# Kernel tuning notes

Measured on AMD Instinct MI355X. Metric: run time of the kernel, lower is better.

The kernel has to match this reference:

```python
import jax, jax.numpy as jnp
import numpy as np

B, IN, H, OUT = 8192, 1024, 1024, 512


def setup_inputs() -> dict:
    key = jax.random.key(0)
    ks = jax.random.split(key, 13)
    s_in = 1.0 / np.sqrt(IN + H)
    s_h = 1.0 / np.sqrt(H)
    return {
        "x": jax.random.normal(ks[0], (B, IN), jnp.float32),
        "h": jax.random.normal(ks[1], (B, H), jnp.float32),
        "c": jax.random.normal(ks[2], (B, H), jnp.float32),
        "Wi": jax.random.normal(ks[3], (IN + H, H), jnp.float32) * s_in,
        "bi": jax.random.normal(ks[4], (H,), jnp.float32) * s_in,
        "Wf": jax.random.normal(ks[5], (IN + H, H), jnp.float32) * s_in,
        "bf": jax.random.normal(ks[6], (H,), jnp.float32) * s_in,
        "Wo": jax.random.normal(ks[7], (IN + H, H), jnp.float32) * s_in,
        "bo": jax.random.normal(ks[8], (H,), jnp.float32) * s_in,
        "Wc": jax.random.normal(ks[9], (IN + H, H), jnp.float32) * s_in,
        "bc": jax.random.normal(ks[10], (H,), jnp.float32) * s_in,
        "Wy": jax.random.normal(ks[11], (H, OUT), jnp.float32) * s_h,
        "by": jax.random.normal(ks[12], (OUT,), jnp.float32) * s_h,
    }


def reference(x, h, c, Wi, bi, Wf, bf, Wo, bo, Wc, bc, Wy, by):
    # combined: [B, IN+H]
    combined = jnp.concatenate([x, h], axis=1)
    # Fuse the four gate matmuls into one [B, IN+H] x [IN+H, 4H] GEMM.
    W_all = jnp.concatenate([Wi, Wf, Wo, Wc], axis=1)        # [IN+H, 4H]
    b_all = jnp.concatenate([bi, bf, bo, bc], axis=0)        # [4H]
    gates = combined @ W_all + b_all                          # [B, 4H]
    gi, gf, go, gc = jnp.split(gates, 4, axis=1)
    i_t = jax.nn.sigmoid(gi)
    f_t = jax.nn.sigmoid(gf)
    o_t = jax.nn.sigmoid(go)
    c_tilde = jnp.tanh(gc)
    c_new = f_t * c + i_t * c_tilde
    h_new = o_t * jnp.tanh(c_new)
    y_hat = h_new @ Wy + by                                   # [B, OUT]
    return (y_hat, (h_new, c_new))
```

## Files before the change

### kernel.cpp

```cpp
#include <hip/hip_runtime.h>
#include <hip/hip_bf16.h>
#include <stdint.h>

#define B_ 8192
#define IN_ 1024
#define H_ 1024
#define OUT_ 512
#define KC 2048
#define N4 4096

typedef __bf16 bf16_t;
typedef __bf16 bf16x8 __attribute__((ext_vector_type(8)));
typedef float f32x4 __attribute__((ext_vector_type(4)));

__device__ __forceinline__ void gload_lds16(const void* g, void* l) {
  __builtin_amdgcn_global_load_lds(
      (const __attribute__((address_space(1))) uint32_t*)g,
      (__attribute__((address_space(3))) uint32_t*)l, 16, 0, 0);
}

__device__ __forceinline__ float fsigmoid(float x) {
  return __builtin_amdgcn_rcpf(1.0f + __expf(-x));
}
__device__ __forceinline__ float ftanh(float x) {
  return 2.0f * __builtin_amdgcn_rcpf(1.0f + __expf(-2.0f * x)) - 1.0f;
}


__global__ __launch_bounds__(256) void pack_combined(
    const float* __restrict__ x, const float* __restrict__ h,
    bf16_t* __restrict__ out) {
  const int row = blockIdx.x;
  const int j = threadIdx.x * 8;
  const float* src = (j < IN_) ? (x + (size_t)row * IN_ + j)
                               : (h + (size_t)row * H_ + (j - IN_));
  float4 a = ((const float4*)src)[0];
  float4 b = ((const float4*)src)[1];
  bf16x8 v;
  v[0] = (bf16_t)a.x; v[1] = (bf16_t)a.y; v[2] = (bf16_t)a.z; v[3] = (bf16_t)a.w;
  v[4] = (bf16_t)b.x; v[5] = (bf16_t)b.y; v[6] = (bf16_t)b.z; v[7] = (bf16_t)b.w;
  *(bf16x8*)(out + (size_t)row * KC + j) = v;
}

__global__ __launch_bounds__(256) void transpose_pack(
    const float* __restrict__ src, bf16_t* __restrict__ dst, int K, int N,
    int RS, int RO) {
  __shared__ float tile[64][65];
  const int k0 = blockIdx.y * 64, n0 = blockIdx.x * 64;
  const int t = threadIdx.x;
  const int tr = t >> 4, tc4 = (t & 15) * 4;
#pragma unroll
  for (int r = 0; r < 4; ++r) {
    const int k = tr + r * 16;
    float4 v = *(const float4*)(src + (size_t)(k0 + k) * N + n0 + tc4);
    tile[k][tc4] = v.x; tile[k][tc4 + 1] = v.y;
    tile[k][tc4 + 2] = v.z; tile[k][tc4 + 3] = v.w;
  }
  __syncthreads();
  const int nr = t >> 3, kc8 = (t & 7) * 8;
#pragma unroll
  for (int r = 0; r < 2; ++r) {
    const int n = nr + r * 32;
    bf16x8 v;
#pragma unroll
    for (int q = 0; q < 8; ++q) v[q] = (bf16_t)tile[kc8 + q][n];
    *(bf16x8*)(dst + (size_t)((n0 + n) * RS + RO) * K + k0 + kc8) = v;
  }
}

__global__ __launch_bounds__(512) void gemm1_8ph(
    const bf16_t* __restrict__ A, const bf16_t* __restrict__ Bt,
    const float* __restrict__ c_in,
    const float* __restrict__ bi, const float* __restrict__ bfg,
    const float* __restrict__ bo, const float* __restrict__ bc,
    float* __restrict__ h_out, float* __restrict__ c_out,
    bf16_t* __restrict__ hb) {
  constexpr int K = KC;
  constexpr int NT = K / 64;
  __shared__ char lds[131072];

  const int tid = threadIdx.x;
  const int lane = tid & 63;
  const int w = tid >> 6;
  const int wr = w >> 2, wc = w & 3;
  const int l15 = lane & 15, l4 = lane >> 4;

  const int wg = blockIdx.x;
  const int swz = (wg & 7) * 64 + (wg >> 3);
  const int bx = swz >> 5;
  const int by = swz & 31;
  const int m0 = by * 256, n0 = bx * 256;

  const int jrow = lane >> 2;
  const int jcol = ((lane & 3) * 16) ^ ((lane >> 5) << 5);
  const char* Asrc = (const char*)A + (size_t)(m0 + w * 16 + jrow) * (K * 2) + jcol;
  const char* Bsrc = (const char*)Bt + (size_t)(n0 + w * 16 + jrow) * (K * 2) + jcol;
  char* ldsA = lds;
  char* ldsB = lds + 32768;
  const int wchunk = w * 2048;

#define STG_A(buf, h, tt) do {                                            \
    gload_lds16(Asrc + (size_t)(h) * 128 * (K * 2) + (size_t)(tt) * 128,  \
                ldsA + (buf) * 65536 + (h) * 16384 + wchunk);             \
    gload_lds16(Asrc + (size_t)(h) * 128 * (K * 2) + (size_t)(tt) * 128 + 64, \
                ldsA + (buf) * 65536 + (h) * 16384 + wchunk + 1024);      \
  } while (0)
#define STG_B(buf, h, tt) do {                                            \
    gload_lds16(Bsrc + (size_t)(h) * 128 * (K * 2) + (size_t)(tt) * 128,  \
                ldsB + (buf) * 65536 + (h) * 16384 + wchunk);             \
    gload_lds16(Bsrc + (size_t)(h) * 128 * (K * 2) + (size_t)(tt) * 128 + 64, \
                ldsB + (buf) * 65536 + (h) * 16384 + wchunk + 1024);      \
  } while (0)

  const int rdoff = l15 * 64 + ((l4 * 16) ^ ((l15 >> 3) << 5));
  const char* ldsArd = lds + wr * 16384 + rdoff;
  const char* ldsBrd = lds + 32768 + (wc >> 1) * 16384 + (wc & 1) * 8192 + rdoff;

  f32x4 acc[8][4] = {};
  bf16x8 fa[4][2], fb[4][2];

#define MFMA_Q(MIBASE, NIBASE)                                                \
  do {                                                                        \
    __builtin_amdgcn_s_setprio(1);                                            \
    _Pragma("unroll") for (int kk = 0; kk < 2; ++kk)                          \
        _Pragma("unroll") for (int mi = 0; mi < 4; ++mi)                      \
            _Pragma("unroll") for (int ni = 0; ni < 2; ++ni)                  \
                acc[(MIBASE) + mi][(NIBASE) + ni] =                           \
                    __builtin_amdgcn_mfma_f32_16x16x32_bf16(                  \
                        fa[mi][kk], fb[(NIBASE) + ni][kk],                    \
                        acc[(MIBASE) + mi][(NIBASE) + ni], 0, 0, 0);          \
    __builtin_amdgcn_s_setprio(0);                                            \
  } while (0)

  STG_B(0, 0, 0); STG_A(0, 0, 0); STG_A(0, 1, 0); STG_B(0, 1, 0);
  STG_B(1, 0, 1); STG_A(1, 0, 1); STG_A(1, 1, 1);
  asm volatile("s_waitcnt vmcnt(6)" ::: "memory");
  __builtin_amdgcn_s_barrier();

  for (int t = 0; t < NT; ++t) {
    const int buf = t & 1;
    const int nbuf = buf ^ 1;
    const char* ard = ldsArd + buf * 65536;
    const char* brd = ldsBrd + buf * 65536;
    const bool st1 = (t + 1 < NT);
    const bool st2 = (t + 2 < NT);

#pragma unroll
    for (int mi = 0; mi < 4; ++mi)
#pragma unroll
      for (int kk = 0; kk < 2; ++kk)
        fa[mi][kk] = *(const bf16x8*)(ard + mi * 2048 + kk * 1024);
#pragma unroll
    for (int ni = 0; ni < 2; ++ni)
#pragma unroll
      for (int kk = 0; kk < 2; ++kk)
        fb[ni][kk] = *(const bf16x8*)(brd + ni * 2048 + kk * 1024);
    if (st1) STG_B(nbuf, 1, t + 1);
    __builtin_amdgcn_s_barrier();
    MFMA_Q(0, 0);
    __builtin_amdgcn_s_barrier();

#pragma unroll
    for (int ni = 2; ni < 4; ++ni)
#pragma unroll
      for (int kk = 0; kk < 2; ++kk)
        fb[ni][kk] = *(const bf16x8*)(brd + ni * 2048 + kk * 1024);
    __builtin_amdgcn_s_barrier();
    MFMA_Q(0, 2);
    __builtin_amdgcn_s_barrier();

#pragma unroll
    for (int mi = 0; mi < 4; ++mi)
#pragma unroll
      for (int kk = 0; kk < 2; ++kk)
        fa[mi][kk] = *(const bf16x8*)(ard + (mi + 4) * 2048 + kk * 1024);
    if (st2) STG_B(buf, 0, t + 2);
    __builtin_amdgcn_s_barrier();
    MFMA_Q(4, 0);
    __builtin_amdgcn_s_barrier();

    if (st2) { STG_A(buf, 0, t + 2); STG_A(buf, 1, t + 2); }
    __builtin_amdgcn_s_barrier();
    MFMA_Q(4, 2);
    if (st2) asm volatile("s_waitcnt vmcnt(6)" ::: "memory");
    else     asm volatile("s_waitcnt vmcnt(0)" ::: "memory");
    __builtin_amdgcn_s_barrier();
  }

  const int hc0 = n0 >> 2;
  float* ldsF = (float*)lds;
  const int ehc = tid & 63;
  const int err0 = (tid >> 6) * 8;
  const float bI = bi[hc0 + ehc];
  const float bF = bfg[hc0 + ehc];
  const float bO = bo[hc0 + ehc];
  const float bC = bc[hc0 + ehc];

  for (int ch = 0; ch < 4; ++ch) {
    __builtin_amdgcn_s_barrier();
    if (wr == (ch >> 1)) {
      const int mib = (ch & 1) * 4;
#pragma unroll
      for (int mi = 0; mi < 4; ++mi)
#pragma unroll
        for (int ni = 0; ni < 4; ++ni) {
          const int col = wc * 64 + ni * 16 + l15;
          const int hc = col >> 2, g = col & 3;
#pragma unroll
          for (int q = 0; q < 4; ++q) {
            const int rr = mi * 16 + l4 * 4 + q;
            ldsF[rr * 256 + ((hc ^ rr) * 4) + g] = acc[mib + mi][ni][q];
          }
        }
    }
    __builtin_amdgcn_s_barrier();
#pragma unroll
    for (int r = 0; r < 8; ++r) {
      const int rr = err0 + r;
      f32x4 gq = *(const f32x4*)&ldsF[rr * 256 + ((ehc ^ rr) * 4)];
      const size_t gidx = (size_t)(m0 + ch * 64 + rr) * H_ + hc0 + ehc;
      float I = fsigmoid(gq[0] + bI);
      float F = fsigmoid(gq[1] + bF);
      float O = fsigmoid(gq[2] + bO);
      float Ct = ftanh(gq[3] + bC);
      float cn = F * c_in[gidx] + I * Ct;
      float hn = O * ftanh(cn);
      c_out[gidx] = cn;
      h_out[gidx] = hn;
      hb[gidx] = (bf16_t)hn;
    }
  }
#undef STG_A
#undef STG_B
#undef MFMA_Q
}

__global__ __launch_bounds__(256) void gemm_bt_f32(
    const bf16_t* __restrict__ A, const bf16_t* __restrict__ Bt,
    float* __restrict__ Cout, const float* __restrict__ bias,
    int M, int N, int K) {
  __shared__ bf16_t As[128 * 64];
  __shared__ bf16_t Bs[128 * 64];
  const int tid = threadIdx.x;
  const int lane = tid & 63;
  const int wave = tid >> 6;
  const int m0 = blockIdx.y * 128;
  const int n0 = blockIdx.x * 128;
  const int wr = wave >> 1, wc = wave & 1;
  const int l15 = lane & 15, l4 = lane >> 4;

  f32x4 acc[4][4] = {};

  const int srow = tid >> 3;
  const int skel = (tid & 7) * 8;
  const size_t aBase = (size_t)(m0 + srow) * K + skel;
  const size_t bBase = (size_t)(n0 + srow) * K + skel;
  char* aL = (char*)As + wave * 1024;
  char* bL = (char*)Bs + wave * 1024;

  for (int kt = 0; kt < K; kt += 64) {
    __syncthreads();
#pragma unroll
    for (int i = 0; i < 4; ++i) {
      gload_lds16(A + aBase + (size_t)i * 32 * K + kt, aL + i * 4096);
      gload_lds16(Bt + bBase + (size_t)i * 32 * K + kt, bL + i * 4096);
    }
    __syncthreads();
#pragma unroll
    for (int kk = 0; kk < 2; ++kk) {
      bf16x8 af[4], bq[4];
#pragma unroll
      for (int mi = 0; mi < 4; ++mi)
        af[mi] = *(const bf16x8*)((const char*)As +
                 (wr * 64 + mi * 16 + l15) * 128 + kk * 64 + l4 * 16);
#pragma unroll
      for (int ni = 0; ni < 4; ++ni)
        bq[ni] = *(const bf16x8*)((const char*)Bs +
                 (wc * 64 + ni * 16 + l15) * 128 + kk * 64 + l4 * 16);
#pragma unroll
      for (int mi = 0; mi < 4; ++mi)
#pragma unroll
        for (int ni = 0; ni < 4; ++ni)
          acc[mi][ni] = __builtin_amdgcn_mfma_f32_16x16x32_bf16(
              af[mi], bq[ni], acc[mi][ni], 0, 0, 0);
    }
  }

  const int col = n0 + wc * 64 + l15;
  const int row0 = m0 + wr * 64 + l4 * 4;
#pragma unroll
  for (int ni = 0; ni < 4; ++ni) {
    const float bv = bias[col + ni * 16];
#pragma unroll
    for (int mi = 0; mi < 4; ++mi)
#pragma unroll
      for (int q = 0; q < 4; ++q)
        Cout[(size_t)(row0 + mi * 16 + q) * N + col + ni * 16] =
            acc[mi][ni][q] + bv;
  }
}

extern "C" void kernel_launch(void* const* d_in, const int* in_sizes, int n_in,
                              void* d_out, int out_size, void* d_ws,
                              size_t ws_size, hipStream_t stream) {
  const float* x = (const float*)d_in[0];
  const float* h = (const float*)d_in[1];
  const float* c = (const float*)d_in[2];
  const float* Wi = (const float*)d_in[3];
  const float* bi = (const float*)d_in[4];
  const float* Wf = (const float*)d_in[5];
  const float* bfg = (const float*)d_in[6];
  const float* Wo = (const float*)d_in[7];
  const float* bo = (const float*)d_in[8];
  const float* Wc = (const float*)d_in[9];
  const float* bc = (const float*)d_in[10];
  const float* Wy = (const float*)d_in[11];
  const float* by = (const float*)d_in[12];

  char* ws = (char*)d_ws;
  bf16_t* combined = (bf16_t*)ws;
  bf16_t* Wt = (bf16_t*)(ws + 33554432);
  bf16_t* Wyt = (bf16_t*)(ws + 33554432 + 16777216);
  bf16_t* hb = (bf16_t*)(ws + 33554432 + 16777216 + 1048576);

  float* y_out = (float*)d_out;
  float* h_out = y_out + (size_t)B_ * OUT_;
  float* c_out = h_out + (size_t)B_ * H_;

  pack_combined<<<dim3(B_), dim3(256), 0, stream>>>(x, h, combined);
  const float* Wg[4] = {Wi, Wf, Wo, Wc};
  for (int g = 0; g < 4; ++g)
    transpose_pack<<<dim3(H_ / 64, KC / 64), dim3(256), 0, stream>>>(
        Wg[g], Wt, KC, H_, 4, g);
  transpose_pack<<<dim3(OUT_ / 64, H_ / 64), dim3(256), 0, stream>>>(
      Wy, Wyt, H_, OUT_, 1, 0);

  gemm1_8ph<<<dim3((B_ / 256) * (N4 / 256)), dim3(512), 0, stream>>>(
      combined, Wt, c, bi, bfg, bo, bc, h_out, c_out, hb);

  gemm_bt_f32<<<dim3(OUT_ / 128, B_ / 128), dim3(256), 0, stream>>>(
      hb, Wyt, y_out, by, B_, OUT_, H_);
}
```

Before: 212.2 us.

## Simplify GEMM1 main loop to a single-stage prefetch and merge gate transposes

Replaces the 8-phase, barrier-heavy ping-pong schedule in the main gate GEMM with a simpler loop. Each iteration reads all A/B fragments from LDS, issues every global-to-LDS load for the next tile, runs 64 MFMAs in two halves, then waits for the loads and does one barrier. This removes the many intra-iteration barriers and the two-tile-ahead staging, at the cost of less fine-grained overlap and more fragment registers held at once. It also fuses the four per-gate weight transpose launches into a single 3D-grid launch to cut launch overhead.

```diff
diff --git a/kernel.cpp b/kernel.cpp
--- a/kernel.cpp
+++ b/kernel.cpp
@@ -42,9 +42,37 @@
   *(bf16x8*)(out + (size_t)row * KC + j) = v;
 }
 
+__global__ __launch_bounds__(256) void transpose_pack4(
+    const float* __restrict__ Wi, const float* __restrict__ Wf,
+    const float* __restrict__ Wo, const float* __restrict__ Wc,
+    bf16_t* __restrict__ dst) {
+  const int g = blockIdx.z;
+  const float* src = (g == 0) ? Wi : (g == 1) ? Wf : (g == 2) ? Wo : Wc;
+  __shared__ float tile[64][65];
+  const int k0 = blockIdx.y * 64, n0 = blockIdx.x * 64;
+  const int t = threadIdx.x;
+  const int tr = t >> 4, tc4 = (t & 15) * 4;
+#pragma unroll
+  for (int r = 0; r < 4; ++r) {
+    const int k = tr + r * 16;
+    float4 v = *(const float4*)(src + (size_t)(k0 + k) * H_ + n0 + tc4);
+    tile[k][tc4] = v.x; tile[k][tc4 + 1] = v.y;
+    tile[k][tc4 + 2] = v.z; tile[k][tc4 + 3] = v.w;
+  }
+  __syncthreads();
+  const int nr = t >> 3, kc8 = (t & 7) * 8;
+#pragma unroll
+  for (int r = 0; r < 2; ++r) {
+    const int n = nr + r * 32;
+    bf16x8 v;
+#pragma unroll
+    for (int q = 0; q < 8; ++q) v[q] = (bf16_t)tile[kc8 + q][n];
+    *(bf16x8*)(dst + (size_t)((n0 + n) * 4 + g) * KC + k0 + kc8) = v;
+  }
+}
+
 __global__ __launch_bounds__(256) void transpose_pack(
-    const float* __restrict__ src, bf16_t* __restrict__ dst, int K, int N,
-    int RS, int RO) {
+    const float* __restrict__ src, bf16_t* __restrict__ dst, int K, int N) {
   __shared__ float tile[64][65];
   const int k0 = blockIdx.y * 64, n0 = blockIdx.x * 64;
   const int t = threadIdx.x;
@@ -64,7 +92,7 @@
     bf16x8 v;
 #pragma unroll
     for (int q = 0; q < 8; ++q) v[q] = (bf16_t)tile[kc8 + q][n];
-    *(bf16x8*)(dst + (size_t)((n0 + n) * RS + RO) * K + k0 + kc8) = v;
+    *(bf16x8*)(dst + (size_t)(n0 + n) * K + k0 + kc8) = v;
   }
 }
 
@@ -117,24 +145,10 @@
   const char* ldsBrd = lds + 32768 + (wc >> 1) * 16384 + (wc & 1) * 8192 + rdoff;
 
   f32x4 acc[8][4] = {};
-  bf16x8 fa[4][2], fb[4][2];
-
-#define MFMA_Q(MIBASE, NIBASE)                                                \
-  do {                                                                        \
-    __builtin_amdgcn_s_setprio(1);                                            \
-    _Pragma("unroll") for (int kk = 0; kk < 2; ++kk)                          \
-        _Pragma("unroll") for (int mi = 0; mi < 4; ++mi)                      \
-            _Pragma("unroll") for (int ni = 0; ni < 2; ++ni)                  \
-                acc[(MIBASE) + mi][(NIBASE) + ni] =                           \
-                    __builtin_amdgcn_mfma_f32_16x16x32_bf16(                  \
-                        fa[mi][kk], fb[(NIBASE) + ni][kk],                    \
-                        acc[(MIBASE) + mi][(NIBASE) + ni], 0, 0, 0);          \
-    __builtin_amdgcn_s_setprio(0);                                            \
-  } while (0)
-
-  STG_B(0, 0, 0); STG_A(0, 0, 0); STG_A(0, 1, 0); STG_B(0, 1, 0);
-  STG_B(1, 0, 1); STG_A(1, 0, 1); STG_A(1, 1, 1);
-  asm volatile("s_waitcnt vmcnt(6)" ::: "memory");
+  bf16x8 falo[4][2], fahi[4][2], fb[4][2];
+
+  STG_B(0, 0, 0); STG_B(0, 1, 0); STG_A(0, 0, 0); STG_A(0, 1, 0);
+  asm volatile("s_waitcnt vmcnt(0)" ::: "memory");
   __builtin_amdgcn_s_barrier();
 
   for (int t = 0; t < NT; ++t) {
@@ -143,47 +157,52 @@
     const char* ard = ldsArd + buf * 65536;
     const char* brd = ldsBrd + buf * 65536;
     const bool st1 = (t + 1 < NT);
-    const bool st2 = (t + 2 < NT);
 
 #pragma unroll
     for (int mi = 0; mi < 4; ++mi)
 #pragma unroll
       for (int kk = 0; kk < 2; ++kk)
-        fa[mi][kk] = *(const bf16x8*)(ard + mi * 2048 + kk * 1024);
-#pragma unroll
-    for (int ni = 0; ni < 2; ++ni)
+        falo[mi][kk] = *(const bf16x8*)(ard + mi * 2048 + kk * 1024);
+#pragma unroll
+    for (int ni = 0; ni < 4; ++ni)
 #pragma unroll
       for (int kk = 0; kk < 2; ++kk)
         fb[ni][kk] = *(const bf16x8*)(brd + ni * 2048 + kk * 1024);
-    if (st1) STG_B(nbuf, 1, t + 1);
-    __builtin_amdgcn_s_barrier();
-    MFMA_Q(0, 0);
-    __builtin_amdgcn_s_barrier();
-
-#pragma unroll
-    for (int ni = 2; ni < 4; ++ni)
+
+    if (st1) {
+      STG_B(nbuf, 0, t + 1); STG_B(nbuf, 1, t + 1);
+      STG_A(nbuf, 0, t + 1); STG_A(nbuf, 1, t + 1);
+    }
+
+#pragma unroll
+    for (int mi = 0; mi < 4; ++mi)
 #pragma unroll
       for (int kk = 0; kk < 2; ++kk)
-        fb[ni][kk] = *(const bf16x8*)(brd + ni * 2048 + kk * 1024);
-    __builtin_amdgcn_s_barrier();
-    MFMA_Q(0, 2);
-    __builtin_amdgcn_s_barrier();
-
-#pragma unroll
-    for (int mi = 0; mi < 4; ++mi)
-#pragma unroll
-      for (int kk = 0; kk < 2; ++kk)
-        fa[mi][kk] = *(const bf16x8*)(ard + (mi + 4) * 2048 + kk * 1024);
-    if (st2) STG_B(buf, 0, t + 2);
-    __builtin_amdgcn_s_barrier();
-    MFMA_Q(4, 0);
-    __builtin_amdgcn_s_barrier();
-
-    if (st2) { STG_A(buf, 0, t + 2); STG_A(buf, 1, t + 2); }
-    __builtin_amdgcn_s_barrier();
-    MFMA_Q(4, 2);
-    if (st2) asm volatile("s_waitcnt vmcnt(6)" ::: "memory");
-    else     asm volatile("s_waitcnt vmcnt(0)" ::: "memory");
+        fahi[mi][kk] = *(const bf16x8*)(ard + (mi + 4) * 2048 + kk * 1024);
+
+    __builtin_amdgcn_s_setprio(1);
+#pragma unroll
+    for (int kk = 0; kk < 2; ++kk)
+#pragma unroll
+      for (int mi = 0; mi < 4; ++mi)
+#pragma unroll
+        for (int ni = 0; ni < 4; ++ni)
+          acc[mi][ni] = __builtin_amdgcn_mfma_f32_16x16x32_bf16(
+              falo[mi][kk], fb[ni][kk], acc[mi][ni], 0, 0, 0);
+    __builtin_amdgcn_s_setprio(0);
+
+    __builtin_amdgcn_s_setprio(1);
+#pragma unroll
+    for (int kk = 0; kk < 2; ++kk)
+#pragma unroll
+      for (int mi = 0; mi < 4; ++mi)
+#pragma unroll
+        for (int ni = 0; ni < 4; ++ni)
+          acc[mi + 4][ni] = __builtin_amdgcn_mfma_f32_16x16x32_bf16(
+              fahi[mi][kk], fb[ni][kk], acc[mi + 4][ni], 0, 0, 0);
+    __builtin_amdgcn_s_setprio(0);
+
+    if (st1) asm volatile("s_waitcnt vmcnt(0)" ::: "memory");
     __builtin_amdgcn_s_barrier();
   }
 
@@ -232,7 +251,6 @@
   }
 #undef STG_A
 #undef STG_B
-#undef MFMA_Q
 }
 
 __global__ __launch_bounds__(256) void gemm_bt_f32(
@@ -328,12 +346,10 @@
   float* c_out = h_out + (size_t)B_ * H_;
 
   pack_combined<<<dim3(B_), dim3(256), 0, stream>>>(x, h, combined);
-  const float* Wg[4] = {Wi, Wf, Wo, Wc};
-  for (int g = 0; g < 4; ++g)
-    transpose_pack<<<dim3(H_ / 64, KC / 64), dim3(256), 0, stream>>>(
-        Wg[g], Wt, KC, H_, 4, g);
+  transpose_pack4<<<dim3(H_ / 64, KC / 64, 4), dim3(256), 0, stream>>>(
+      Wi, Wf, Wo, Wc, Wt);
   transpose_pack<<<dim3(OUT_ / 64, H_ / 64), dim3(256), 0, stream>>>(
-      Wy, Wyt, H_, OUT_, 1, 0);
+      Wy, Wyt, H_, OUT_);
 
   gemm1_8ph<<<dim3((B_ / 256) * (N4 / 256)), dim3(512), 0, stream>>>(
       combined, Wt, c, bi, bfg, bo, bc, h_out, c_out, hb);
```

Measured after the change: 197.5 us. -6.9%, faster.

## Merge gate weight transposes into one launch and halve epilogue LDS passes

Applied to the files above, without the earlier changes.

The four per-gate transpose_pack launches become a single 3D-grid launch, cutting launch overhead. The gemm1 epilogue now has both wave-row groups stage their accumulators into separate 64KB LDS halves at once, so it needs two store/compute passes instead of four with idle waves. An explicit lgkmcnt wait is also added before the first barrier in the main loop. These trade a few barriers and launches for more LDS use per pass.

```diff
diff --git a/kernel.cpp b/kernel.cpp
--- a/kernel.cpp
+++ b/kernel.cpp
@@ -42,9 +42,37 @@
   *(bf16x8*)(out + (size_t)row * KC + j) = v;
 }
 
+__global__ __launch_bounds__(256) void transpose_pack4(
+    const float* __restrict__ Wi, const float* __restrict__ Wf,
+    const float* __restrict__ Wo, const float* __restrict__ Wc,
+    bf16_t* __restrict__ dst) {
+  const int g = blockIdx.z;
+  const float* src = (g == 0) ? Wi : (g == 1) ? Wf : (g == 2) ? Wo : Wc;
+  __shared__ float tile[64][65];
+  const int k0 = blockIdx.y * 64, n0 = blockIdx.x * 64;
+  const int t = threadIdx.x;
+  const int tr = t >> 4, tc4 = (t & 15) * 4;
+#pragma unroll
+  for (int r = 0; r < 4; ++r) {
+    const int k = tr + r * 16;
+    float4 v = *(const float4*)(src + (size_t)(k0 + k) * H_ + n0 + tc4);
+    tile[k][tc4] = v.x; tile[k][tc4 + 1] = v.y;
+    tile[k][tc4 + 2] = v.z; tile[k][tc4 + 3] = v.w;
+  }
+  __syncthreads();
+  const int nr = t >> 3, kc8 = (t & 7) * 8;
+#pragma unroll
+  for (int r = 0; r < 2; ++r) {
+    const int n = nr + r * 32;
+    bf16x8 v;
+#pragma unroll
+    for (int q = 0; q < 8; ++q) v[q] = (bf16_t)tile[kc8 + q][n];
+    *(bf16x8*)(dst + (size_t)((n0 + n) * 4 + g) * KC + k0 + kc8) = v;
+  }
+}
+
 __global__ __launch_bounds__(256) void transpose_pack(
-    const float* __restrict__ src, bf16_t* __restrict__ dst, int K, int N,
-    int RS, int RO) {
+    const float* __restrict__ src, bf16_t* __restrict__ dst, int K, int N) {
   __shared__ float tile[64][65];
   const int k0 = blockIdx.y * 64, n0 = blockIdx.x * 64;
   const int t = threadIdx.x;
@@ -64,7 +92,7 @@
     bf16x8 v;
 #pragma unroll
     for (int q = 0; q < 8; ++q) v[q] = (bf16_t)tile[kc8 + q][n];
-    *(bf16x8*)(dst + (size_t)((n0 + n) * RS + RO) * K + k0 + kc8) = v;
+    *(bf16x8*)(dst + (size_t)(n0 + n) * K + k0 + kc8) = v;
   }
 }
 
@@ -156,6 +184,7 @@
       for (int kk = 0; kk < 2; ++kk)
         fb[ni][kk] = *(const bf16x8*)(brd + ni * 2048 + kk * 1024);
     if (st1) STG_B(nbuf, 1, t + 1);
+    asm volatile("s_waitcnt lgkmcnt(8)" ::: "memory");
     __builtin_amdgcn_s_barrier();
     MFMA_Q(0, 0);
     __builtin_amdgcn_s_barrier();
@@ -188,7 +217,6 @@
   }
 
   const int hc0 = n0 >> 2;
-  float* ldsF = (float*)lds;
   const int ehc = tid & 63;
   const int err0 = (tid >> 6) * 8;
   const float bI = bi[hc0 + ehc];
@@ -196,10 +224,11 @@
   const float bO = bo[hc0 + ehc];
   const float bC = bc[hc0 + ehc];
 
-  for (int ch = 0; ch < 4; ++ch) {
-    __builtin_amdgcn_s_barrier();
-    if (wr == (ch >> 1)) {
-      const int mib = (ch & 1) * 4;
+  for (int p = 0; p < 2; ++p) {
+    __builtin_amdgcn_s_barrier();
+    {
+      float* dst = (float*)(lds + wr * 65536);
+      const int mib = p * 4;
 #pragma unroll
       for (int mi = 0; mi < 4; ++mi)
 #pragma unroll
@@ -209,25 +238,30 @@
 #pragma unroll
           for (int q = 0; q < 4; ++q) {
             const int rr = mi * 16 + l4 * 4 + q;
-            ldsF[rr * 256 + ((hc ^ rr) * 4) + g] = acc[mib + mi][ni][q];
+            dst[rr * 256 + ((hc ^ rr) * 4) + g] = acc[mib + mi][ni][q];
           }
         }
     }
     __builtin_amdgcn_s_barrier();
 #pragma unroll
-    for (int r = 0; r < 8; ++r) {
-      const int rr = err0 + r;
-      f32x4 gq = *(const f32x4*)&ldsF[rr * 256 + ((ehc ^ rr) * 4)];
-      const size_t gidx = (size_t)(m0 + ch * 64 + rr) * H_ + hc0 + ehc;
-      float I = fsigmoid(gq[0] + bI);
-      float F = fsigmoid(gq[1] + bF);
-      float O = fsigmoid(gq[2] + bO);
-      float Ct = ftanh(gq[3] + bC);
-      float cn = F * c_in[gidx] + I * Ct;
-      float hn = O * ftanh(cn);
-      c_out[gidx] = cn;
-      h_out[gidx] = hn;
-      hb[gidx] = (bf16_t)hn;
+    for (int half = 0; half < 2; ++half) {
+      const float* src = (const float*)(lds + half * 65536);
+#pragma unroll
+      for (int r = 0; r < 8; ++r) {
+        const int rr = err0 + r;
+        f32x4 gq = *(const f32x4*)&src[rr * 256 + ((ehc ^ rr) * 4)];
+        const size_t gidx =
+            (size_t)(m0 + half * 128 + p * 64 + rr) * H_ + hc0 + ehc;
+        float I = fsigmoid(gq[0] + bI);
+        float F = fsigmoid(gq[1] + bF);
+        float O = fsigmoid(gq[2] + bO);
+        float Ct = ftanh(gq[3] + bC);
+        float cn = F * c_in[gidx] + I * Ct;
+        float hn = O * ftanh(cn);
+        c_out[gidx] = cn;
+        h_out[gidx] = hn;
+        hb[gidx] = (bf16_t)hn;
+      }
     }
   }
 #undef STG_A
@@ -328,12 +362,10 @@
   float* c_out = h_out + (size_t)B_ * H_;
 
   pack_combined<<<dim3(B_), dim3(256), 0, stream>>>(x, h, combined);
-  const float* Wg[4] = {Wi, Wf, Wo, Wc};
-  for (int g = 0; g < 4; ++g)
-    transpose_pack<<<dim3(H_ / 64, KC / 64), dim3(256), 0, stream>>>(
-        Wg[g], Wt, KC, H_, 4, g);
+  transpose_pack4<<<dim3(H_ / 64, KC / 64, 4), dim3(256), 0, stream>>>(
+      Wi, Wf, Wo, Wc, Wt);
   transpose_pack<<<dim3(OUT_ / 64, H_ / 64), dim3(256), 0, stream>>>(
-      Wy, Wyt, H_, OUT_, 1, 0);
+      Wy, Wyt, H_, OUT_);
 
   gemm1_8ph<<<dim3((B_ / 256) * (N4 / 256)), dim3(512), 0, stream>>>(
       combined, Wt, c, bi, bfg, bo, bc, h_out, c_out, hb);
```

After: 197.4 us. -7.0%, faster.
